# Kernel tuning notes

Measured on AMD Instinct MI355X. Metric: run time of the kernel, lower is better.

The kernel has to match this reference:

```python
import jax, jax.numpy as jnp
import numpy as np

N = 50000
E = 800000
IN_DIM = 64
HID = 64
OUT = 40


def setup_inputs() -> dict:
    key = jax.random.key(0)
    ks = jax.random.split(key, 10)
    x = jax.random.normal(ks[0], (N, IN_DIM), dtype=jnp.float32)
    edge_index = jax.random.randint(ks[1], (2, E), 0, N, dtype=jnp.int64)

    def lin(k, fan_in, fan_out):
        # torch nn.Linear default init: U(-1/sqrt(fan_in), 1/sqrt(fan_in))
        bound = 1.0 / np.sqrt(fan_in)
        kw, kb = jax.random.split(k)
        W = jax.random.uniform(kw, (fan_in, fan_out), minval=-bound, maxval=bound, dtype=jnp.float32)
        b = jax.random.uniform(kb, (fan_out,), minval=-bound, maxval=bound, dtype=jnp.float32)
        return W, b

    W1, b1 = lin(ks[2], IN_DIM, HID)   # conv layer 1
    W2, b2 = lin(ks[3], HID, HID)      # conv layer 2
    Wp1, bp1 = lin(ks[4], HID, HID)    # post_mp linear 1
    Wp2, bp2 = lin(ks[5], HID, OUT)    # post_mp linear 2
    return {"x": x, "edge_index": edge_index,
            "W1": W1, "b1": b1, "W2": W2, "b2": b2,
            "Wp1": Wp1, "bp1": bp1, "Wp2": Wp2, "bp2": bp2}


def _mean_aggregate(h, src, dst, num_nodes):
    # Row-normalized sparse adjacency matmul: out[i] = (1/deg(i)) * sum_{(i,j) in E} h[j]
    # adj[src, dst] = 1/deg(src), where deg(src) = #outgoing edges of src.
    ones = jnp.ones((src.shape[0],), dtype=h.dtype)
    deg = jax.ops.segment_sum(ones, src, num_segments=num_nodes)
    w = 1.0 / deg[src]                         # [E], every src has deg >= 1
    msgs = h[dst] * w[:, None]                 # [E, d] gather + scale
    return jax.ops.segment_sum(msgs, src, num_segments=num_nodes)  # [N, d]


def reference(x, edge_index, W1, b1, W2, b2, Wp1, bp1, Wp2, bp2):
    src = edge_index[0]
    dst = edge_index[1]
    n = x.shape[0]
    # GraphSAGEConvolution layer 1: (dropout=eval noop) linear -> spmm mean-agg -> relu
    h = x @ W1 + b1
    h = _mean_aggregate(h, src, dst, n)
    h = jax.nn.relu(h)
    # GraphSAGEConvolution layer 2
    h = h @ W2 + b2
    h = _mean_aggregate(h, src, dst, n)
    h = jax.nn.relu(h)
    # post_mp: Linear -> (dropout noop) -> Linear
    h = h @ Wp1 + bp1
    h = h @ Wp2 + bp2
    return jax.nn.log_softmax(h, axis=1)
```

## Files before the change

kernel.cpp:

```cpp
#include <hip/hip_runtime.h>
#include <cmath>


typedef _Float16 half_t;
typedef half_t half2_t __attribute__((ext_vector_type(2)));
typedef half_t half4_t __attribute__((ext_vector_type(4)));

#if defined(__has_builtin)
# if __has_builtin(__builtin_amdgcn_fdot2)
#  define FDOT2(a, b, c) __builtin_amdgcn_fdot2((a), (b), (c), false)
# endif
#endif
#ifndef FDOT2
# define FDOT2(a, b, c) fmaf((float)(a)[0], (float)(b)[0], fmaf((float)(a)[1], (float)(b)[1], (c)))
#endif

#define NXCD 8
#define CAP  64
#define EDGE_BLOCKS 1024
#define WS 66

__global__ __launch_bounds__(256) void build_h1(
    const int* __restrict__ src, const int* __restrict__ dst,
    const float* __restrict__ x, const float* __restrict__ W1,
    const float* __restrict__ b1,
    const float* __restrict__ W2, const float* __restrict__ Wp1,
    const float* __restrict__ Wp2,
    half_t* __restrict__ Wt, int* __restrict__ cnt,
    unsigned short* __restrict__ col, half_t* __restrict__ Hh,
    int E, int N)
{
    const int tid = threadIdx.x;

    if (blockIdx.x < EDGE_BLOCKS) {
        int gid = blockIdx.x * 256 + tid;
        if (gid < 3 * 4096) {
            int which = gid >> 12, r = gid & 4095;
            int c = r >> 6, k = r & 63;
            float v;
            if      (which == 0) v = W2[k * 64 + c];
            else if (which == 1) v = Wp1[k * 64 + c];
            else                 v = (c < 40) ? Wp2[k * 40 + c] : 0.f;
            Wt[gid] = (half_t)v;
        }

        const int g     = blockIdx.x & (NXCD - 1);
        const int bpg   = blockIdx.x >> 3;
        const int nbpg  = EDGE_BLOCKS >> 3;
        const int chunk = (N + NXCD - 1) / NXCD;
        const int lo = g * chunk;
        const int hi = min(N, lo + chunk);
        const int4* src4 = (const int4*)src;
        const int4* dst4 = (const int4*)dst;
        const int quads = E >> 2;
        for (int q = bpg * 256 + tid; q < quads; q += nbpg * 256) {
            int4 s4 = src4[q];
            bool any = (s4.x >= lo && s4.x < hi) || (s4.y >= lo && s4.y < hi) ||
                       (s4.z >= lo && s4.z < hi) || (s4.w >= lo && s4.w < hi);
            if (!any) continue;
            int4 d4 = dst4[q];
            if (s4.x >= lo && s4.x < hi) {
                int pos = atomicAdd(&cnt[s4.x], 1);
                if (pos < CAP) col[(size_t)s4.x * CAP + pos] = (unsigned short)d4.x;
            }
            if (s4.y >= lo && s4.y < hi) {
                int pos = atomicAdd(&cnt[s4.y], 1);
                if (pos < CAP) col[(size_t)s4.y * CAP + pos] = (unsigned short)d4.y;
            }
            if (s4.z >= lo && s4.z < hi) {
                int pos = atomicAdd(&cnt[s4.z], 1);
                if (pos < CAP) col[(size_t)s4.z * CAP + pos] = (unsigned short)d4.z;
            }
            if (s4.w >= lo && s4.w < hi) {
                int pos = atomicAdd(&cnt[s4.w], 1);
                if (pos < CAP) col[(size_t)s4.w * CAP + pos] = (unsigned short)d4.w;
            }
        }
        if (blockIdx.x == 0 && tid < (E & 3)) {
            int e = (E & ~3) + tid;
            int s = src[e];
            int pos = atomicAdd(&cnt[s], 1);
            if (pos < CAP) col[(size_t)s * CAP + pos] = (unsigned short)dst[e];
        }
    } else {
        __shared__ half_t xs[16][64];
        const int lane = tid & 63;
        const int wid  = tid >> 6;
        const int row0 = (blockIdx.x - EDGE_BLOCKS) * 16;

        for (int i = tid; i < 16 * 64; i += 256) {
            int rr = row0 + (i >> 6);
            float v = (rr < N) ? x[(size_t)row0 * 64 + i] : 0.f;
            xs[i >> 6][i & 63] = (half_t)v;
        }
        const float bias = b1[lane];
        __syncthreads();

        float acc[4] = {bias, bias, bias, bias};
#pragma unroll 1
        for (int c = 0; c < 4; ++c) {
            half2_t wr[8];
#pragma unroll
            for (int j = 0; j < 8; ++j) {
                float a0 = W1[(c * 16 + 2 * j + 0) * 64 + lane];
                float a1 = W1[(c * 16 + 2 * j + 1) * 64 + lane];
                half2_t h; h[0] = (half_t)a0; h[1] = (half_t)a1;
                wr[j] = h;
            }
#pragma unroll
            for (int r = 0; r < 4; ++r) {
                const half2_t* xp = (const half2_t*)&xs[wid * 4 + r][c * 16];
#pragma unroll
                for (int j = 0; j < 8; ++j) acc[r] = FDOT2(xp[j], wr[j], acc[r]);
            }
        }
#pragma unroll
        for (int r = 0; r < 4; ++r) {
            int grow = row0 + wid * 4 + r;
            if (grow < N) Hh[(size_t)grow * 64 + lane] = (half_t)acc[r];
        }
    }
}

__device__ __forceinline__ void gather_node(const char* __restrict__ Hbytes,
                                            const unsigned short* __restrict__ cbase,
                                            int deg, int grp, int suboff, float* f) {
    const int myo = ((int)cbase[threadIdx.x & 63]) << 7;
    f[0] = f[1] = f[2] = f[3] = 0.f;
    const int full = deg & ~15;
    int e = 0;
    for (; e < full; e += 16) {
        half4_t hacc; hacc[0] = (half_t)0.f; hacc[1] = (half_t)0.f;
        hacc[2] = (half_t)0.f; hacc[3] = (half_t)0.f;
#pragma unroll
        for (int i = 0; i < 4; ++i) {
            int off = __shfl(myo, e + 4 * i + grp);
            hacc += *(const half4_t*)(Hbytes + off + suboff);
        }
        f[0] += (float)hacc[0]; f[1] += (float)hacc[1];
        f[2] += (float)hacc[2]; f[3] += (float)hacc[3];
    }
    if (e < deg) {
        half4_t hacc; hacc[0] = (half_t)0.f; hacc[1] = (half_t)0.f;
        hacc[2] = (half_t)0.f; hacc[3] = (half_t)0.f;
#pragma unroll
        for (int i = 0; i < 4; ++i) {
            int idx = e + 4 * i + grp;
            int off = __shfl(myo, idx & 63);
            if (idx < deg) hacc += *(const half4_t*)(Hbytes + off + suboff);
        }
        f[0] += (float)hacc[0]; f[1] += (float)hacc[1];
        f[2] += (float)hacc[2]; f[3] += (float)hacc[3];
    }
#pragma unroll
    for (int k = 0; k < 4; ++k) {
        f[k] += __shfl_xor(f[k], 16);
        f[k] += __shfl_xor(f[k], 32);
    }
}

__device__ __forceinline__ void stage_w(const half_t* __restrict__ Wt,
                                        half_t* __restrict__ wlds, int tid, int nthr) {
    const unsigned* ws = (const unsigned*)Wt;
    unsigned* wd = (unsigned*)wlds;
    for (int i = tid; i < 2048; i += nthr) {
        int c = i >> 5, kp = i & 31;
        wd[c * (WS / 2) + kp] = ws[i];
    }
}

__global__ __launch_bounds__(512) void fused_gather_gemm(
    const half_t* __restrict__ H, const int* __restrict__ cnt,
    const unsigned short* __restrict__ colb, const half_t* __restrict__ Wt,
    const float* __restrict__ b, half_t* __restrict__ Y, int N)
{
    __shared__ half_t wlds[64 * WS];
    __shared__ __align__(16) half_t xrow[8][64];
    const int tid  = threadIdx.x;
    const int w    = tid >> 6;
    const int lane = tid & 63;
    const int grp  = lane >> 4;
    const int sub  = lane & 15;

    stage_w(Wt, wlds, tid, 512);
    __syncthreads();

    const int node = blockIdx.x * 8 + w;
    if (node >= N) return;

    const int deg = cnt[node];
    float f[4];
    gather_node((const char*)H, colb + (size_t)node * CAP, deg, grp, sub * 8, f);
    if (grp == 0) {
        float inv = (deg > 0) ? 1.f / (float)deg : 0.f;
        half4_t o;
        o[0] = (half_t)fmaxf(f[0] * inv, 0.f);
        o[1] = (half_t)fmaxf(f[1] * inv, 0.f);
        o[2] = (half_t)fmaxf(f[2] * inv, 0.f);
        o[3] = (half_t)fmaxf(f[3] * inv, 0.f);
        ((half4_t*)xrow[w])[sub] = o;
    }

    float a0 = b[lane], a1 = 0.f;
    const half2_t* wl = (const half2_t*)(wlds + (size_t)lane * WS);
    const half2_t* xp = (const half2_t*)xrow[w];
#pragma unroll
    for (int i = 0; i < 16; ++i) {
        a0 = FDOT2(xp[2 * i + 0], wl[2 * i + 0], a0);
        a1 = FDOT2(xp[2 * i + 1], wl[2 * i + 1], a1);
    }
    Y[(size_t)node * 64 + lane] = (half_t)(a0 + a1);
}

__global__ __launch_bounds__(256) void gemm40_softmax(const half_t* __restrict__ H3,
                                                      const half_t* __restrict__ Wt2,
                                                      const float* __restrict__ bp2,
                                                      float* __restrict__ out, int n) {
    __shared__ half_t xs[16][64];
    __shared__ half_t wlds[64 * WS];
    const int tid  = threadIdx.x;
    const int lane = tid & 63;
    const int wid  = tid >> 6;
    const int row0 = blockIdx.x * 16;

    stage_w(Wt2, wlds, tid, 256);
    {
        const half2_t* X2 = (const half2_t*)H3;
        half2_t z; z[0] = (half_t)0.f; z[1] = (half_t)0.f;
        for (int i = tid; i < 16 * 32; i += 256) {
            int rr = row0 + (i >> 5);
            ((half2_t*)xs)[i] = (rr < n) ? X2[(size_t)row0 * 32 + i] : z;
        }
    }
    const float bias2 = (lane < 40) ? bp2[lane] : 0.f;
    __syncthreads();

    float acc[4] = {bias2, bias2, bias2, bias2};
    const half2_t* wl = (const half2_t*)(wlds + (size_t)lane * WS);
#pragma unroll
    for (int c = 0; c < 2; ++c) {
        half2_t wr[16];
#pragma unroll
        for (int i = 0; i < 16; ++i) wr[i] = wl[c * 16 + i];
#pragma unroll
        for (int r = 0; r < 4; ++r) {
            const half2_t* xp = (const half2_t*)&xs[wid * 4 + r][c * 32];
#pragma unroll
            for (int i = 0; i < 16; ++i) acc[r] = FDOT2(xp[i], wr[i], acc[r]);
        }
    }

#pragma unroll
    for (int r = 0; r < 4; ++r) {
        float vm = (lane < 40) ? acc[r] : -INFINITY;
        float m = vm;
#pragma unroll
        for (int o = 32; o; o >>= 1) m = fmaxf(m, __shfl_xor(m, o));
        float e = (lane < 40) ? expf(vm - m) : 0.f;
        float s = e;
#pragma unroll
        for (int o = 32; o; o >>= 1) s += __shfl_xor(s, o);
        float ls = logf(s);
        const int grow = row0 + wid * 4 + r;
        if (grow < n && lane < 40) out[(size_t)grow * 40 + lane] = vm - m - ls;
    }
}

extern "C" void kernel_launch(void* const* d_in, const int* in_sizes, int n_in,
                              void* d_out, int out_size, void* d_ws, size_t ws_size,
                              hipStream_t stream) {
    const float* x   = (const float*)d_in[0];
    const int*   ei  = (const int*)d_in[1];
    const float* W1  = (const float*)d_in[2];
    const float* b1  = (const float*)d_in[3];
    const float* W2  = (const float*)d_in[4];
    const float* b2  = (const float*)d_in[5];
    const float* Wp1 = (const float*)d_in[6];
    const float* bp1 = (const float*)d_in[7];
    const float* Wp2 = (const float*)d_in[8];
    const float* bp2 = (const float*)d_in[9];
    float* out = (float*)d_out;

    const int N = in_sizes[0] / 64;
    const int E = in_sizes[1] / 2;
    const int* src = ei;
    const int* dst = ei + E;

    char*  wsb = (char*)d_ws;
    size_t off = 0;
    auto alloc = [&](size_t bytes) { void* p = wsb + off; off += (bytes + 511) & ~(size_t)511; return p; };
    int*            cnt = (int*)alloc((size_t)N * 4);
    unsigned short* col = (unsigned short*)alloc((size_t)N * CAP * 2);
    half_t*         Wt  = (half_t*)alloc((size_t)3 * 4096 * 2);
    half_t*         Ha  = (half_t*)alloc((size_t)N * 64 * 2);
    half_t*         Hb  = (half_t*)alloc((size_t)N * 64 * 2);
    (void)ws_size; (void)n_in; (void)out_size;

    const int nb16 = (N + 15) / 16;
    const int nb8  = (N + 7) / 8;

    hipMemsetAsync(cnt, 0, (size_t)N * 4, stream);
    build_h1<<<EDGE_BLOCKS + nb16, 256, 0, stream>>>(src, dst, x, W1, b1, W2, Wp1, Wp2,
                                                     Wt, cnt, col, Ha, E, N);
    fused_gather_gemm<<<nb8, 512, 0, stream>>>(Ha, cnt, col, Wt + 0 * 4096, b2, Hb, N);
    fused_gather_gemm<<<nb8, 512, 0, stream>>>(Hb, cnt, col, Wt + 1 * 4096, bp1, Ha, N);
    gemm40_softmax<<<nb16, 256, 0, stream>>>(Ha, Wt + 2 * 4096, bp2, out, N);
}
```

Before: 135.3 us.

## Interleave transposed weights for 128-bit LDS loads and double edge blocks

Changes the pre-transposed half weight layout to an [k/8][col][8] interleave so each lane reads 8 consecutive k-values with a single 128-bit LDS load, replacing the padded (WS=66) row layout and its 32-bit loads. Weight staging becomes a straight uint4 copy, and both GEMM kernels use half8 vector reads for weights and activations. It also doubles EDGE_BLOCKS for the edge-bucketing phase to add parallelism. Wider LDS accesses reduce LDS instruction count, at the cost of relying on the new layout being conflict-free.

```diff
diff --git a/kernel.cpp b/kernel.cpp
--- a/kernel.cpp
+++ b/kernel.cpp
@@ -5,6 +5,7 @@
 typedef _Float16 half_t;
 typedef half_t half2_t __attribute__((ext_vector_type(2)));
 typedef half_t half4_t __attribute__((ext_vector_type(4)));
+typedef half_t half8_t __attribute__((ext_vector_type(8)));
 
 #if defined(__has_builtin)
 # if __has_builtin(__builtin_amdgcn_fdot2)
@@ -17,8 +18,7 @@
 
 #define NXCD 8
 #define CAP  64
-#define EDGE_BLOCKS 1024
-#define WS 66
+#define EDGE_BLOCKS 2048
 
 __global__ __launch_bounds__(256) void build_h1(
     const int* __restrict__ src, const int* __restrict__ dst,
@@ -36,7 +36,8 @@
         int gid = blockIdx.x * 256 + tid;
         if (gid < 3 * 4096) {
             int which = gid >> 12, r = gid & 4095;
-            int c = r >> 6, k = r & 63;
+            int i = r >> 9, c = (r >> 3) & 63, j = r & 7;
+            int k = i * 8 + j;
             float v;
             if      (which == 0) v = W2[k * 64 + c];
             else if (which == 1) v = Wp1[k * 64 + c];
@@ -161,11 +162,26 @@
 
 __device__ __forceinline__ void stage_w(const half_t* __restrict__ Wt,
                                         half_t* __restrict__ wlds, int tid, int nthr) {
-    const unsigned* ws = (const unsigned*)Wt;
-    unsigned* wd = (unsigned*)wlds;
-    for (int i = tid; i < 2048; i += nthr) {
-        int c = i >> 5, kp = i & 31;
-        wd[c * (WS / 2) + kp] = ws[i];
+    const uint4* ws = (const uint4*)Wt;
+    uint4* wd = (uint4*)wlds;
+    for (int i = tid; i < 512; i += nthr) wd[i] = ws[i];
+}
+
+__device__ __forceinline__ void dot64_b128(const half_t* __restrict__ xrow,
+                                           const half_t* __restrict__ wlds,
+                                           int lane, float& a0, float& a1) {
+    const half8_t* wl8 = (const half8_t*)wlds;
+    const half8_t* xp8 = (const half8_t*)xrow;
+#pragma unroll
+    for (int i = 0; i < 8; ++i) {
+        half8_t wv = wl8[i * 64 + lane];
+        half8_t xv = xp8[i];
+        const half2_t* w2 = (const half2_t*)&wv;
+        const half2_t* x2 = (const half2_t*)&xv;
+        a0 = FDOT2(x2[0], w2[0], a0);
+        a1 = FDOT2(x2[1], w2[1], a1);
+        a0 = FDOT2(x2[2], w2[2], a0);
+        a1 = FDOT2(x2[3], w2[3], a1);
     }
 }
 
@@ -174,7 +190,7 @@
     const unsigned short* __restrict__ colb, const half_t* __restrict__ Wt,
     const float* __restrict__ b, half_t* __restrict__ Y, int N)
 {
-    __shared__ half_t wlds[64 * WS];
+    __shared__ __align__(16) half_t wlds[4096];
     __shared__ __align__(16) half_t xrow[8][64];
     const int tid  = threadIdx.x;
     const int w    = tid >> 6;
@@ -202,13 +218,7 @@
     }
 
     float a0 = b[lane], a1 = 0.f;
-    const half2_t* wl = (const half2_t*)(wlds + (size_t)lane * WS);
-    const half2_t* xp = (const half2_t*)xrow[w];
-#pragma unroll
-    for (int i = 0; i < 16; ++i) {
-        a0 = FDOT2(xp[2 * i + 0], wl[2 * i + 0], a0);
-        a1 = FDOT2(xp[2 * i + 1], wl[2 * i + 1], a1);
-    }
+    dot64_b128(xrow[w], wlds, lane, a0, a1);
     Y[(size_t)node * 64 + lane] = (half_t)(a0 + a1);
 }
 
@@ -216,8 +226,8 @@
                                                       const half_t* __restrict__ Wt2,
                                                       const float* __restrict__ bp2,
                                                       float* __restrict__ out, int n) {
-    __shared__ half_t xs[16][64];
-    __shared__ half_t wlds[64 * WS];
+    __shared__ __align__(16) half_t xs[16][64];
+    __shared__ __align__(16) half_t wlds[4096];
     const int tid  = threadIdx.x;
     const int lane = tid & 63;
     const int wid  = tid >> 6;
@@ -235,24 +245,28 @@
     const float bias2 = (lane < 40) ? bp2[lane] : 0.f;
     __syncthreads();
 
-    float acc[4] = {bias2, bias2, bias2, bias2};
-    const half2_t* wl = (const half2_t*)(wlds + (size_t)lane * WS);
-#pragma unroll
-    for (int c = 0; c < 2; ++c) {
-        half2_t wr[16];
-#pragma unroll
-        for (int i = 0; i < 16; ++i) wr[i] = wl[c * 16 + i];
+    float a0[4] = {bias2, bias2, bias2, bias2};
+    float a1[4] = {0.f, 0.f, 0.f, 0.f};
+    const half8_t* wl8 = (const half8_t*)wlds;
+#pragma unroll
+    for (int i = 0; i < 8; ++i) {
+        half8_t wv = wl8[i * 64 + lane];
+        const half2_t* w2 = (const half2_t*)&wv;
 #pragma unroll
         for (int r = 0; r < 4; ++r) {
-            const half2_t* xp = (const half2_t*)&xs[wid * 4 + r][c * 32];
-#pragma unroll
-            for (int i = 0; i < 16; ++i) acc[r] = FDOT2(xp[i], wr[i], acc[r]);
+            half8_t xv = ((const half8_t*)&xs[wid * 4 + r][0])[i];
+            const half2_t* x2 = (const half2_t*)&xv;
+            a0[r] = FDOT2(x2[0], w2[0], a0[r]);
+            a1[r] = FDOT2(x2[1], w2[1], a1[r]);
+            a0[r] = FDOT2(x2[2], w2[2], a0[r]);
+            a1[r] = FDOT2(x2[3], w2[3], a1[r]);
         }
     }
 
 #pragma unroll
     for (int r = 0; r < 4; ++r) {
-        float vm = (lane < 40) ? acc[r] : -INFINITY;
+        float acc = a0[r] + a1[r];
+        float vm = (lane < 40) ? acc : -INFINITY;
         float m = vm;
 #pragma unroll
         for (int o = 32; o; o >>= 1) m = fmaxf(m, __shfl_xor(m, o));
```

After: 128.0 us, median of 2. 1.06x faster.
